# Performance work log

Hardware: AMD Instinct MI355X
Metric: run time of the kernel (lower is better)

The kernel has to match this reference:

```python
import jax, jax.numpy as jnp
import numpy as np

B, S, W = 32, 128, 16
E, CD, H, P = 256, 64, 512, 256
V, CV, NC = 50000, 256, 6
CK, WK = 8, 64  # merged char/word conv kernel sizes


def conv1d(x, w, b):
    # x: [N, Cin, L], w: [Cout, Cin, K] -> [N, Cout, L-K+1] (VALID)
    y = jax.lax.conv_general_dilated(x, w, (1,), 'VALID',
                                     dimension_numbers=('NCH', 'OIH', 'NCH'))
    return y + b[None, :, None]


def setup_inputs() -> dict:
    key = jax.random.key(0)
    ks = iter(jax.random.split(key, 40))
    nrm = lambda shape: jax.random.normal(next(ks), shape, dtype=jnp.float32) * 0.05
    return {
        'seq': jax.random.randint(next(ks), (B, S), 0, V),
        'seq_char': jax.random.randint(next(ks), (B, S, W), 0, CV),
        'classes': jnp.arange(NC, dtype=jnp.int32).reshape(NC, 1),
        'embed_w': nrm((V, E)),
        'char_embed_w': nrm((CV, CD)),
        'class_embed_w': nrm((NC, E)),
        'char_conv_w': nrm((CD, CD, CK)), 'char_conv_b': nrm((CD,)),
        'word_conv_w': nrm((E, E + CD, WK)), 'word_conv_b': nrm((E,)),
        'f_Wih': nrm((4 * H, E + CD)), 'f_Whh': nrm((4 * H, H)), 'f_b': nrm((4 * H,)),
        'b_Wih': nrm((4 * H, E + CD)), 'b_Whh': nrm((4 * H, H)), 'b_b': nrm((4 * H,)),
        'attend': nrm((E, 2 * H)),
        'd_Wih': nrm((6 * H, E + 2 * H)), 'd_Whh': nrm((6 * H, 2 * H)),
        'd_bih': nrm((6 * H,)), 'd_bhh': nrm((6 * H,)),
        'proj_w': nrm((P, 2 * H)), 'proj_b': nrm((P,)),
        'cls_w': nrm((2, P)), 'cls_b': nrm((2,)),
    }


def reference(seq, seq_char, classes, embed_w, char_embed_w, class_embed_w,
              char_conv_w, char_conv_b, word_conv_w, word_conv_b,
              f_Wih, f_Whh, f_b, b_Wih, b_Whh, b_b, attend,
              d_Wih, d_Whh, d_bih, d_bhh, proj_w, proj_b, cls_w, cls_b):
    # eval-mode forward (dropout p=0.01 is identity at eval time)
    Bq, Sq = seq.shape
    pad_mask = (seq > 0).astype(jnp.float32)            # [B,S]
    word_e = jnp.tanh(embed_w[seq])                     # [B,S,E]
    # char CNN: all char convs share kernel size -> merged into one conv
    ce = char_embed_w[seq_char]                         # [B,S,W,CD]
    ce = ce.reshape(Bq * Sq, W, CD).transpose(0, 2, 1)  # [B*S, CD, W]
    char_feat = jnp.tanh(conv1d(ce, char_conv_w, char_conv_b).mean(-1).reshape(Bq, Sq, CD))
    x = jnp.concatenate([word_e, char_feat], -1)        # [B,S,E+CD]
    # word CNN over full sequence -> [B,E]
    conv_seq = jnp.tanh(conv1d(x.transpose(0, 2, 1), word_conv_w, word_conv_b).mean(-1))
    # BiLSTM; backward direction uses seq_emb[-i], i.e. order [0, S-1, ..., 1] (as in original)
    xs = x.transpose(1, 0, 2)                           # [S,B,E+CD]
    xs_b = xs[(-jnp.arange(Sq)) % Sq]

    def lstm_scan(Wih, Whh, b, inputs):
        def step(carry, xt):
            h, c = carry
            g = xt @ Wih.T + h @ Whh.T + b
            i, f, gg, o = jnp.split(g, 4, axis=-1)
            c = jax.nn.sigmoid(f) * c + jax.nn.sigmoid(i) * jnp.tanh(gg)
            h = jax.nn.sigmoid(o) * jnp.tanh(c)
            return (h, c), h
        h0 = jnp.zeros((Bq, H), x.dtype)
        _, hs = jax.lax.scan(step, (h0, h0), inputs)
        return hs

    fouts = lstm_scan(f_Wih, f_Whh, f_b, xs)            # [S,B,H]
    bouts = lstm_scan(b_Wih, b_Whh, b_b, xs_b)[::-1]    # reversed, as in original
    seq_repr = jnp.concatenate([fouts, bouts], -1)      # [S,B,2H]
    h0 = seq_repr[-1]                                   # decoder init state [B,2H]
    seq_repr = seq_repr.transpose(1, 0, 2)              # [B,S,2H]
    # class attention: the expanded attn rows are identical across positions,
    # so sum over dim 1 of the [B,S,S] bmm equals S * tanh(a_c) . seq_repr[b,t]
    a = jnp.tanh(jnp.tanh(class_embed_w[classes[:, 0]])) @ attend   # [C,2H]
    scores = Sq * jnp.einsum('ch,bth->cbt', jnp.tanh(a), seq_repr)  # [C,B,S]
    scores = scores * pad_mask[None]
    att_ctx = jnp.einsum('cbt,bth->cbh', jnp.tanh(scores), seq_repr)  # [C,B,2H]

    def gru_step(h, ctx):
        inp = jnp.concatenate([conv_seq, ctx], -1)      # [B, E+2H]
        gi = inp @ d_Wih.T + d_bih
        gh = h @ d_Whh.T + d_bhh
        ir, iz, inn = jnp.split(gi, 3, -1)
        hr, hz, hn = jnp.split(gh, 3, -1)
        r = jax.nn.sigmoid(ir + hr)
        z = jax.nn.sigmoid(iz + hz)
        n = jnp.tanh(inn + r * hn)
        h_new = jnp.tanh((1 - z) * n + z * h)           # post-tanh state fed back (as in original)
        logits = (h_new @ proj_w.T + proj_b) @ cls_w.T + cls_b
        return h_new, jax.nn.log_softmax(logits, -1)

    _, outs = jax.lax.scan(gru_step, h0, att_ctx)       # [C,B,2]
    return outs
```

## Files before the change

kernel.cpp:

```cpp
#include <hip/hip_runtime.h>

typedef __bf16 bf16_t;
typedef __bf16 bf16x8 __attribute__((ext_vector_type(8)));
typedef float f32x4 __attribute__((ext_vector_type(4)));
typedef unsigned u32x4 __attribute__((ext_vector_type(4)));
typedef unsigned long long u64;

static constexpr int BB = 32, SS = 128, WW = 16, EE = 256, CDm = 64, HH = 512, PP = 256;
static constexpr int EC = 320;
static constexpr int H2 = 1024;
static constexpr int G6 = 3072;
static constexpr int NKT = 28;
static constexpr int NKTX = 12;

__device__ __forceinline__ float sigm(float x){ return 1.f/(1.f + expf(-x)); }

#define ALOAD(p)    __hip_atomic_load((p),  __ATOMIC_RELAXED, __HIP_MEMORY_SCOPE_AGENT)
#define ASTORE(p,v) __hip_atomic_store((p),(v),__ATOMIC_RELAXED, __HIP_MEMORY_SCOPE_AGENT)

template<bool LLC>
__device__ __forceinline__ unsigned ld_flag(const unsigned* p){
  unsigned r;
  if constexpr (LLC)
    asm volatile("global_load_dword %0, %1, off sc0 sc1\n\ts_waitcnt vmcnt(0)"
                 : "=&v"(r) : "v"(p) : "memory");
  else
    asm volatile("global_load_dword %0, %1, off sc0\n\ts_waitcnt vmcnt(0)"
                 : "=&v"(r) : "v"(p) : "memory");
  return r;
}
template<bool LLC>
__device__ __forceinline__ void ld16(u32x4& d, const void* p){
  if constexpr (LLC)
    asm volatile("global_load_dwordx4 %0, %1, off sc0 sc1" : "=&v"(d) : "v"(p) : "memory");
  else
    asm volatile("global_load_dwordx4 %0, %1, off sc0"     : "=&v"(d) : "v"(p) : "memory");
}
template<bool LLC>
__device__ __forceinline__ void st32(unsigned* p, unsigned v){
  if constexpr (LLC)
    asm volatile("global_store_dword %0, %1, off sc0 sc1" :: "v"(p), "v"(v) : "memory");
  else
    asm volatile("global_store_dword %0, %1, off sc0"     :: "v"(p), "v"(v) : "memory");
}
__device__ __forceinline__ void vm_drain(){
  asm volatile("s_waitcnt vmcnt(0)" ::: "memory");
  __builtin_amdgcn_sched_barrier(0);
}

__global__ void k_embed_cbar(const int* __restrict__ seq, const float* __restrict__ embed_w,
                             const int* __restrict__ seq_char, const float* __restrict__ cemb,
                             float* __restrict__ x, float* __restrict__ mask,
                             float* __restrict__ cbar){
  int bs = blockIdx.x; int tid = threadIdx.x;
  int wid = seq[bs];
  x[(size_t)bs*EC + tid] = tanhf(embed_w[(size_t)wid*EE + tid]);
  if (tid == 0) mask[bs] = (wid > 0) ? 1.f : 0.f;
  if (tid < 64){
    int c = tid;
    float ce[WW];
    #pragma unroll
    for (int p = 0; p < WW; ++p){
      int id = seq_char[bs*WW + p];
      ce[p] = cemb[(size_t)id*CDm + c];
    }
    #pragma unroll
    for (int k = 0; k < 8; ++k){
      float s = 0.f;
      #pragma unroll
      for (int p = 0; p < 9; ++p) s += ce[k+p];
      cbar[(size_t)bs*512 + c*8 + k] = s * (1.f/9.f);
    }
  }
}

__global__ __launch_bounds__(64) void k_xbar(const float* __restrict__ x, float* __restrict__ xbar){
  __shared__ float xl[64][129];
  int gid = blockIdx.x*64 + threadIdx.x;
  int b = gid / EC, c = gid % EC;
  int tl = threadIdx.x;
  for (int t = 0; t < SS; ++t) xl[tl][t] = x[((size_t)b*SS + t)*EC + c];
  float s = 0.f;
  for (int t = 0; t < 65; ++t) s += xl[tl][t];
  const float inv = 1.f/65.f;
  float* o = &xbar[(size_t)(b*EC + c)*64];
  o[0] = s*inv;
  for (int k = 1; k < 64; ++k){ s += xl[tl][k+64] - xl[tl][k-1]; o[k] = s*inv; }
}

template<int BM,int BN,int TM,int TN>
__global__ __launch_bounds__(256) void k_gemm(const float* __restrict__ A,
    const float* __restrict__ Wm, float* __restrict__ part,
    int M, int N, int K, int kslice){
  __shared__ float As[32][BM+4];
  __shared__ float Ws[32][BN+4];
  const int tid = threadIdx.x;
  const int tx = tid & 15, ty = tid >> 4;
  const int m0 = blockIdx.x*BM, n0 = blockIdx.y*BN, ks = blockIdx.z;
  const int kb = ks*kslice;
  float acc[TM][TN];
  #pragma unroll
  for (int i = 0; i < TM; ++i)
    #pragma unroll
    for (int j = 0; j < TN; ++j) acc[i][j] = 0.f;
  for (int kt = 0; kt < kslice; kt += 32){
    constexpr int AIT = (BM*8)/256;
    #pragma unroll
    for (int it = 0; it < AIT; ++it){
      int ch = tid + it*256;
      int r = ch >> 3, kc = (ch & 7)*4;
      float4 v = *(const float4*)(A + (size_t)(m0+r)*K + kb + kt + kc);
      As[kc+0][r]=v.x; As[kc+1][r]=v.y; As[kc+2][r]=v.z; As[kc+3][r]=v.w;
    }
    constexpr int WIT = (BN*8)/256;
    #pragma unroll
    for (int it = 0; it < WIT; ++it){
      int ch = tid + it*256;
      int r = ch >> 3, kc = (ch & 7)*4;
      float4 v = *(const float4*)(Wm + (size_t)(n0+r)*K + kb + kt + kc);
      Ws[kc+0][r]=v.x; Ws[kc+1][r]=v.y; Ws[kc+2][r]=v.z; Ws[kc+3][r]=v.w;
    }
    __syncthreads();
    #pragma unroll
    for (int kk = 0; kk < 32; ++kk){
      float a[TM], wv[TN];
      #pragma unroll
      for (int i = 0; i < TM; ++i) a[i] = As[kk][ty*TM+i];
      #pragma unroll
      for (int j = 0; j < TN; ++j) wv[j] = Ws[kk][tx*TN+j];
      #pragma unroll
      for (int i = 0; i < TM; ++i)
        #pragma unroll
        for (int j = 0; j < TN; ++j) acc[i][j] = fmaf(a[i], wv[j], acc[i][j]);
    }
    __syncthreads();
  }
  #pragma unroll
  for (int i = 0; i < TM; ++i){
    int row = m0 + ty*TM + i;
    #pragma unroll
    for (int j = 0; j < TN; ++j){
      int col = n0 + tx*TN + j;
      part[((size_t)ks*M + row)*N + col] = acc[i][j];
    }
  }
}

__global__ __launch_bounds__(256) void k_cgemm(const float* __restrict__ A,
    const float* __restrict__ Wm, const float* __restrict__ bias, float* __restrict__ x){
  __shared__ float As[32][36];
  __shared__ float Ws[32][68];
  const int tid = threadIdx.x;
  const int tx = tid & 15, ty = tid >> 4;
  const int m0 = blockIdx.x*32;
  float acc[2][4];
  #pragma unroll
  for (int i = 0; i < 2; ++i)
    #pragma unroll
    for (int j = 0; j < 4; ++j) acc[i][j] = 0.f;
  for (int kt = 0; kt < 512; kt += 32){
    {
      int r = tid >> 3, kc = (tid & 7)*4;
      float4 v = *(const float4*)(A + (size_t)(m0+r)*512 + kt + kc);
      As[kc+0][r]=v.x; As[kc+1][r]=v.y; As[kc+2][r]=v.z; As[kc+3][r]=v.w;
    }
    #pragma unroll
    for (int it = 0; it < 2; ++it){
      int ch = tid + it*256;
      int r = ch >> 3, kc = (ch & 7)*4;
      float4 v = *(const float4*)(Wm + (size_t)r*512 + kt + kc);
      Ws[kc+0][r]=v.x; Ws[kc+1][r]=v.y; Ws[kc+2][r]=v.z; Ws[kc+3][r]=v.w;
    }
    __syncthreads();
    #pragma unroll
    for (int kk = 0; kk < 32; ++kk){
      float a[2], wv[4];
      a[0] = As[kk][ty*2]; a[1] = As[kk][ty*2+1];
      #pragma unroll
      for (int j = 0; j < 4; ++j) wv[j] = Ws[kk][tx*4+j];
      #pragma unroll
      for (int i = 0; i < 2; ++i)
        #pragma unroll
        for (int j = 0; j < 4; ++j) acc[i][j] = fmaf(a[i], wv[j], acc[i][j]);
    }
    __syncthreads();
  }
  #pragma unroll
  for (int i = 0; i < 2; ++i){
    int row = m0 + ty*2 + i;
    #pragma unroll
    for (int j = 0; j < 4; ++j){
      int col = tx*4 + j;
      x[(size_t)row*EC + 256 + col] = tanhf(acc[i][j] + bias[col]);
    }
  }
}

__global__ __launch_bounds__(64) void k_fin(const float* __restrict__ part,
    const float* __restrict__ bias, float* __restrict__ out,
    int M, int N, int KS, int ldc, int act){
  int col = blockIdx.x*64 + threadIdx.x;
  int row = blockIdx.y;
  float v = bias ? bias[col] : 0.f;
  for (int ks = 0; ks < KS; ++ks) v += part[((size_t)ks*M + row)*N + col];
  if (act) v = tanhf(v);
  out[(size_t)row*ldc + col] = v;
}

__global__ __launch_bounds__(64) void k_packw(const float* __restrict__ fWih, const float* __restrict__ fWhh,
    const float* __restrict__ bWih, const float* __restrict__ bWhh, bf16_t* __restrict__ Wp){
  int id = blockIdx.x;
  int kt = id % NKT; id /= NKT;
  int slice = id % 32; int dir = id / 32;
  int l = threadIdx.x;
  const float* Whh = dir ? bWhh : fWhh;
  const float* Wih = dir ? bWih : fWih;
  int krow = (l >> 4)*8;
  for (int nt = 0; nt < 4; ++nt){
    int row = nt*512 + slice*16 + (l & 15);
    bf16_t* dst = &Wp[((((size_t)(dir*32+slice)*NKT + kt)*4 + nt)*64 + l)*8];
    if (kt < 16){
      const float* src = &Whh[(size_t)row*512 + kt*32 + krow];
      #pragma unroll
      for (int r = 0; r < 8; ++r) dst[r] = (bf16_t)src[r];
    } else {
      int kx = (kt-16)*32 + krow;
      if (kx + 8 <= 320){
        const float* src = &Wih[(size_t)row*320 + kx];
        #pragma unroll
        for (int r = 0; r < 8; ++r) dst[r] = (bf16_t)src[r];
      } else {
        #pragma unroll
        for (int r = 0; r < 8; ++r) dst[r] = (bf16_t)0.f;
      }
    }
  }
}

__global__ __launch_bounds__(64) void k_packdw(const float* __restrict__ W, bf16_t* __restrict__ Wo){
  int id = blockIdx.x;
  int kt = id % 32; id /= 32;
  int nt = id % 3;  int wg = id / 3;
  int l = threadIdx.x;
  int col = nt*1024 + wg*16 + (l & 15);
  int k0 = kt*32 + (l >> 4)*8;
  bf16_t* dst = Wo + (((size_t)(wg*3 + nt)*32 + kt)*64 + l)*8;
  const float* src = W + (size_t)col*1024 + k0;
  #pragma unroll
  for (int r = 0; r < 8; ++r) dst[r] = (bf16_t)src[r];
}

__global__ __launch_bounds__(64) void k_packpw(const float* __restrict__ W, bf16_t* __restrict__ Wo){
  int id = blockIdx.x;
  int kt = id & 31, wg = id >> 5;
  int l = threadIdx.x;
  int col = wg*16 + (l & 15);
  int k0 = kt*32 + (l >> 4)*8;
  bf16_t* dst = Wo + (((size_t)wg*32 + kt)*64 + l)*8;
  const float* src = W + (size_t)col*1024 + k0;
  #pragma unroll
  for (int r = 0; r < 8; ++r) dst[r] = (bf16_t)src[r];
}

__global__ __launch_bounds__(64) void k_packx(const float* __restrict__ x, bf16_t* __restrict__ xp){
  int id = blockIdx.x;
  int ktx = id % NKTX; id /= NKTX;
  int mt = id & 1; int t = id >> 1;
  int l = threadIdx.x;
  int b = (l & 15) + 16*mt;
  int c = ktx*32 + (l >> 4)*8;
  bf16_t* dst = &xp[(((size_t)t*2 + mt)*NKTX + ktx)*64*8 + (size_t)l*8];
  if (c + 8 <= EC){
    const float* src = &x[((size_t)b*SS + t)*EC + c];
    #pragma unroll
    for (int r = 0; r < 8; ++r) dst[r] = (bf16_t)src[r];
  } else {
    #pragma unroll
    for (int r = 0; r < 8; ++r) dst[r] = (bf16_t)0.f;
  }
}

__global__ __launch_bounds__(256) void k_zero(unsigned int* __restrict__ base, int n){
  int i = blockIdx.x*256 + threadIdx.x;
  if (i < n) ASTORE(base + i, 0u);
}

__global__ __launch_bounds__(64) void k_hprep(const float* __restrict__ seq_repr,
                                              bf16_t* __restrict__ hdp){
  int mt = blockIdx.x >> 5, kt = blockIdx.x & 31, l = threadIdx.x;
  int b = mt*16 + (l & 15);
  int jb = kt*32 + (l >> 4)*8;
  const float* src = &seq_repr[((size_t)b*SS + 127)*H2 + jb];
  unsigned* dst = (unsigned*)(hdp + (((size_t)mt*32 + kt)*64 + l)*8);
  #pragma unroll
  for (int p = 0; p < 4; ++p){
    unsigned pk = (unsigned)__builtin_bit_cast(unsigned short, (bf16_t)src[2*p])
                | ((unsigned)__builtin_bit_cast(unsigned short, (bf16_t)src[2*p+1]) << 16);
    ASTORE(dst + p, pk);
  }
}

template<bool LLC>
__device__ void lstm_body(const bf16_t* __restrict__ Wp, const bf16_t* __restrict__ xp,
    bf16_t* __restrict__ hp, const float* __restrict__ fb, const float* __restrict__ bb,
    float* __restrict__ seq_repr, unsigned* __restrict__ lf,
    int dir, int slice, int tid, bf16_t* Wl, float (*red)[32][65],
    float* bias_l, float (*c_l)[32]){
  const int wv = tid >> 6, lane = tid & 63;
  {
    const uint4* src = (const uint4*)(Wp + ((size_t)(dir*32 + slice))*NKT*4*64*8);
    uint4* dst = (uint4*)Wl;
    for (int i = tid; i < NKT*4*64*8/8; i += 256) dst[i] = src[i];
  }
  if (tid < 64){
    const float* bv = dir ? bb : fb;
    bias_l[tid] = bv[(tid >> 4)*512 + slice*16 + (tid & 15)];
  }
  ((float*)c_l)[tid]       = 0.f;
  ((float*)c_l)[tid + 256] = 0.f;
  __syncthreads();

  for (int t = 0; t < SS; ++t){
    const int ph = t & 1;
    const int s = dir ? ((SS - t) & 127) : t;
    f32x4 acc[2][4];
    f32x4 zero = {0.f,0.f,0.f,0.f};
    #pragma unroll
    for (int m = 0; m < 2; ++m)
      #pragma unroll
      for (int n = 0; n < 4; ++n) acc[m][n] = zero;

    const bf16_t* xb = xp + (size_t)s*2*NKTX*64*8;
    bf16x8 ax[3][2];
    #pragma unroll
    for (int i = 0; i < 3; ++i){
      int ktx = wv*3 + i;
      #pragma unroll
      for (int m = 0; m < 2; ++m)
        ax[i][m] = *reinterpret_cast<const bf16x8*>(xb + (((size_t)m*NKTX + ktx)*64 + lane)*8);
    }
    #pragma unroll
    for (int i = 0; i < 3; ++i){
      int kt = 16 + wv*3 + i;
      #pragma unroll
      for (int nt = 0; nt < 4; ++nt){
        bf16x8 Bf = *reinterpret_cast<const bf16x8*>(&Wl[(((size_t)kt*4 + nt)*64 + lane)*8]);
        acc[0][nt] = __builtin_amdgcn_mfma_f32_16x16x32_bf16(ax[i][0], Bf, acc[0][nt], 0, 0, 0);
        acc[1][nt] = __builtin_amdgcn_mfma_f32_16x16x32_bf16(ax[i][1], Bf, acc[1][nt], 0, 0, 0);
      }
    }
    if (t > 0 && lane < 8){
      int prod = dir*32 + (wv + 4*(lane >> 1))*2 + (lane & 1);
      const unsigned* fp = lf + prod*16;
      unsigned tgt = (unsigned)t;
      for(;;){
        unsigned v = ld_flag<LLC>(fp);
        if (__ballot(v < tgt) == 0ull) break;
      }
    }
    const bf16_t* hb_ = hp + ((size_t)(ph*2 + dir))*2*16*64*8;
    u32x4 hr[4][2];
    #pragma unroll
    for (int i = 0; i < 4; ++i){
      int kt = wv + 4*i;
      #pragma unroll
      for (int m = 0; m < 2; ++m)
        ld16<LLC>(hr[i][m], hb_ + (((size_t)m*16 + kt)*64 + lane)*8);
    }
    vm_drain();
    #pragma unroll
    for (int i = 0; i < 4; ++i){
      int kt = wv + 4*i;
      bf16x8 a0 = __builtin_bit_cast(bf16x8, hr[i][0]);
      bf16x8 a1 = __builtin_bit_cast(bf16x8, hr[i][1]);
      #pragma unroll
      for (int nt = 0; nt < 4; ++nt){
        bf16x8 Bf = *reinterpret_cast<const bf16x8*>(&Wl[(((size_t)kt*4 + nt)*64 + lane)*8]);
        acc[0][nt] = __builtin_amdgcn_mfma_f32_16x16x32_bf16(a0, Bf, acc[0][nt], 0, 0, 0);
        acc[1][nt] = __builtin_amdgcn_mfma_f32_16x16x32_bf16(a1, Bf, acc[1][nt], 0, 0, 0);
      }
    }
    {
      int r0 = (lane >> 4)*4, cc = lane & 15;
      #pragma unroll
      for (int m = 0; m < 2; ++m)
        #pragma unroll
        for (int n = 0; n < 4; ++n)
          #pragma unroll
          for (int e = 0; e < 4; ++e)
            red[wv][m*16 + r0 + e][n*16 + cc] = acc[m][n][e];
    }
    __syncthreads();
    {
      int b = tid & 31, jjp = tid >> 5;
      float hv[2];
      #pragma unroll
      for (int u2 = 0; u2 < 2; ++u2){
        int jj = jjp*2 + u2;
        float gi_ = bias_l[jj],     gf_ = bias_l[16+jj];
        float gg_ = bias_l[32+jj],  go_ = bias_l[48+jj];
        #pragma unroll
        for (int w2 = 0; w2 < 4; ++w2){
          gi_ += red[w2][b][jj];      gf_ += red[w2][b][16+jj];
          gg_ += red[w2][b][32+jj];   go_ += red[w2][b][48+jj];
        }
        float ii = sigm(gi_), ff = sigm(gf_), g2 = tanhf(gg_), oo = sigm(go_);
        float c = ff*c_l[jj][b] + ii*g2;
        c_l[jj][b] = c;
        hv[u2] = oo*tanhf(c);
      }
      int j0 = slice*16 + jjp*2;
      int s_out = dir ? (127 - t) : t;
      float2 st; st.x = hv[0]; st.y = hv[1];
      *(float2*)&seq_repr[((size_t)b*SS + s_out)*H2 + dir*HH + j0] = st;
      int mt = b >> 4, kth = j0 >> 5, ln = (b & 15) + 16*((j0 >> 3) & 3), rg = j0 & 7;
      unsigned pk = (unsigned)__builtin_bit_cast(unsigned short, (bf16_t)hv[0])
                  | ((unsigned)__builtin_bit_cast(unsigned short, (bf16_t)hv[1]) << 16);
      unsigned* dst = (unsigned*)(hp +
          ((((size_t)((ph^1)*2 + dir)*2 + mt)*16 + kth)*64 + ln)*8 + rg);
      st32<LLC>(dst, pk);
    }
    asm volatile("s_waitcnt vmcnt(0)" ::: "memory");
    __syncthreads();
    if (tid == 0)
      st32<LLC>(lf + (dir*32 + slice)*16, (unsigned)(t+1));
  }
}

__global__ __launch_bounds__(256, 1) void k_lstm(const bf16_t* __restrict__ Wp,
    const bf16_t* __restrict__ xp, bf16_t* __restrict__ hp,
    const float* __restrict__ fb, const float* __restrict__ bb,
    float* __restrict__ seq_repr, unsigned* __restrict__ lf,
    unsigned* __restrict__ xcc_tab, unsigned* __restrict__ modep){
  const int blk = blockIdx.x;
  const int tid = threadIdx.x;
  __shared__ __align__(16) bf16_t Wl[NKT*4*64*8];
  __shared__ float red[4][32][65];
  __shared__ float bias_l[64];
  __shared__ float c_l[16][32];
  __shared__ unsigned mode_s;

  unsigned xcc;
  asm volatile("s_getreg_b32 %0, hwreg(HW_REG_XCC_ID)" : "=s"(xcc));
  if (tid == 0) ASTORE(xcc_tab + blk, xcc + 1u);
  if (blk == 0){
    unsigned* tabl = (unsigned*)red;
    unsigned v = 0; int spins = 0;
    for (;;){
      v = ALOAD(xcc_tab + tid);
      if (v != 0u || spins >= 200000) break;
      ++spins; __builtin_amdgcn_s_sleep(2);
    }
    tabl[tid] = v;
    __syncthreads();
    if (tid == 0){
      unsigned mode = 1;
      unsigned c0 = tabl[0], c1 = tabl[1];
      if (c0 == 0u || c1 == 0u) mode = 2;
      for (int k = 0; k < 32; ++k)
        if (tabl[8*k] != c0 || tabl[8*k + 1] != c1) mode = 2;
      ASTORE(modep, mode);
      mode_s = mode;
    }
    __syncthreads();
  } else {
    if (tid == 0){
      unsigned m;
      while ((m = ALOAD(modep)) == 0u) __builtin_amdgcn_s_sleep(2);
      mode_s = m;
    }
    __syncthreads();
  }
  const unsigned mode = mode_s;
  int dir, slice; bool worker;
  if (mode == 1){ worker = (blk & 7) < 2; dir = blk & 7; slice = blk >> 3; }
  else          { worker = blk < 64;      dir = blk >> 5; slice = blk & 31; }
  if (!worker) return;
  if (mode == 1)
    lstm_body<false>(Wp, xp, hp, fb, bb, seq_repr, lf, dir, slice, tid, Wl, red, bias_l, c_l);
  else
    lstm_body<true >(Wp, xp, hp, fb, bb, seq_repr, lf, dir, slice, tid, Wl, red, bias_l, c_l);
}

__global__ __launch_bounds__(256) void k_ta(const int* __restrict__ classes,
    const float* __restrict__ cls_emb, const float* __restrict__ attend, float* __restrict__ ta){
  int c = blockIdx.x;
  __shared__ float t2[EE];
  int tid = threadIdx.x;
  int ci = classes[c];
  t2[tid] = tanhf(tanhf(cls_emb[(size_t)ci*EE + tid]));
  __syncthreads();
  for (int r = 0; r < 4; ++r){
    int h = r*256 + tid;
    float acc = 0.f;
    for (int e = 0; e < EE; ++e) acc = fmaf(t2[e], attend[(size_t)e*H2 + h], acc);
    ta[c*H2 + h] = tanhf(acc);
  }
}

__global__ __launch_bounds__(256) void k_ctx(const float* __restrict__ ta,
    const float* __restrict__ seq_repr, const float* __restrict__ mask, float* __restrict__ ctx){
  int c = blockIdx.x, b = blockIdx.y;
  __shared__ float ta_l[H2];
  __shared__ float ps[128][2];
  __shared__ float sc[128];
  int tid = threadIdx.x;
  for (int i = tid; i < H2; i += 256) ta_l[i] = ta[c*H2 + i];
  __syncthreads();
  {
    int tt = tid >> 1, half = tid & 1;
    const float* row = &seq_repr[((size_t)b*SS + tt)*H2 + half*512];
    const float* tl = &ta_l[half*512];
    float p = 0.f;
    for (int i = 0; i < 512; i += 4){
      float4 v = *(const float4*)&row[i];
      p = fmaf(tl[i], v.x, p);   p = fmaf(tl[i+1], v.y, p);
      p = fmaf(tl[i+2], v.z, p); p = fmaf(tl[i+3], v.w, p);
    }
    ps[tt][half] = p;
  }
  __syncthreads();
  if (tid < 128){
    float s = (ps[tid][0] + ps[tid][1]) * 128.f * mask[b*SS + tid];
    sc[tid] = tanhf(s);
  }
  __syncthreads();
  {
    int h = tid*4;
    float4 a = {0.f,0.f,0.f,0.f};
    for (int t = 0; t < SS; ++t){
      float s = sc[t];
      float4 v = *(const float4*)&seq_repr[((size_t)b*SS + t)*H2 + h];
      a.x = fmaf(s, v.x, a.x); a.y = fmaf(s, v.y, a.y);
      a.z = fmaf(s, v.z, a.z); a.w = fmaf(s, v.w, a.w);
    }
    *(float4*)&ctx[((size_t)c*BB + b)*H2 + h] = a;
  }
}

__global__ __launch_bounds__(256) void k_gemmgi(const float* __restrict__ conv_seq,
    const float* __restrict__ ctx, const float* __restrict__ Wm, float* __restrict__ part){
  __shared__ float As[32][68];
  __shared__ float Ws[32][68];
  const int tid = threadIdx.x;
  const int tx = tid & 15, ty = tid >> 4;
  const int m0 = blockIdx.x*64, n0 = blockIdx.y*64, ks = blockIdx.z;
  const int kb = ks*320;
  float acc[4][4];
  #pragma unroll
  for (int i = 0; i < 4; ++i)
    #pragma unroll
    for (int j = 0; j < 4; ++j) acc[i][j] = 0.f;
  for (int kt = 0; kt < 320; kt += 32){
    #pragma unroll
    for (int it = 0; it < 2; ++it){
      int ch = tid + it*256;
      int r = ch >> 3, kc = (ch & 7)*4;
      int row = m0 + r;
      int cc2 = row >> 5, bb2 = row & 31;
      int k4 = kb + kt + kc;
      const float* ap = (k4 < 256) ? (conv_seq + bb2*256 + k4)
                                   : (ctx + ((size_t)(cc2*BB) + bb2)*H2 + (k4 - 256));
      float4 v = *(const float4*)ap;
      As[kc+0][r]=v.x; As[kc+1][r]=v.y; As[kc+2][r]=v.z; As[kc+3][r]=v.w;
    }
    #pragma unroll
    for (int it = 0; it < 2; ++it){
      int ch = tid + it*256;
      int r = ch >> 3, kc = (ch & 7)*4;
      float4 v = *(const float4*)(Wm + (size_t)(n0+r)*1280 + kb + kt + kc);
      Ws[kc+0][r]=v.x; Ws[kc+1][r]=v.y; Ws[kc+2][r]=v.z; Ws[kc+3][r]=v.w;
    }
    __syncthreads();
    #pragma unroll
    for (int kk = 0; kk < 32; ++kk){
      float a[4], wv[4];
      #pragma unroll
      for (int i = 0; i < 4; ++i) a[i] = As[kk][ty*4+i];
      #pragma unroll
      for (int j = 0; j < 4; ++j) wv[j] = Ws[kk][tx*4+j];
      #pragma unroll
      for (int i = 0; i < 4; ++i)
        #pragma unroll
        for (int j = 0; j < 4; ++j) acc[i][j] = fmaf(a[i], wv[j], acc[i][j]);
    }
    __syncthreads();
  }
  #pragma unroll
  for (int i = 0; i < 4; ++i){
    int row = m0 + ty*4 + i;
    #pragma unroll
    for (int j = 0; j < 4; ++j){
      int col = n0 + tx*4 + j;
      part[((size_t)ks*192 + row)*G6 + col] = acc[i][j];
    }
  }
}

__global__ __launch_bounds__(256, 1) void k_dec(
    const bf16_t* __restrict__ Whp, const bf16_t* __restrict__ Ppw,
    const float* __restrict__ gi, const float* __restrict__ d_bhh,
    const float* __restrict__ seq_repr,
    const float* __restrict__ proj_b, const float* __restrict__ cls_w,
    const float* __restrict__ cls_b, bf16_t* __restrict__ hdp,
    float* __restrict__ pl, unsigned int* __restrict__ dfh,
    unsigned int* __restrict__ dfpl, float* __restrict__ out){
  const int wg = blockIdx.x;
  const int tid = threadIdx.x;
  const int wv = tid >> 6, lane = tid & 63;
  __shared__ __align__(16) bf16_t Wl[3*32*64*8];
  __shared__ float red[4][32][49];
  __shared__ float plred[8][32][2];
  __shared__ float cv[2];
  {
    const uint4* src = (const uint4*)(Whp + (size_t)wg*3*32*64*8);
    uint4* dst = (uint4*)Wl;
    for (int i = tid; i < 3*32*64*8/8; i += 256) dst[i] = src[i];
  }
  const int b = tid & 31, jp = tid >> 5;
  const int j0 = wg*16 + jp*2;
  float hold[2];
  hold[0] = seq_repr[((size_t)b*SS + 127)*H2 + j0];
  hold[1] = seq_repr[((size_t)b*SS + 127)*H2 + j0 + 1];
  float bhh[3][2];
  #pragma unroll
  for (int g = 0; g < 3; ++g){
    bhh[g][0] = d_bhh[g*1024 + j0];
    bhh[g][1] = d_bhh[g*1024 + j0 + 1];
  }
  __syncthreads();
  union HU { unsigned long long u[2]; bf16x8 v; };
  const int r0 = (lane >> 4)*4, cc = lane & 15;

  for (int c = 0; c < 6; ++c){
    if (c > 0){
      const unsigned int* fp = dfh + lane*16;
      unsigned tgt = (unsigned)c;
      for(;;){
        unsigned v = ALOAD(fp);
        if (__ballot(v < tgt) == 0ull) break;
      }
    }
    f32x4 acc[2][3];
    f32x4 zero = {0.f,0.f,0.f,0.f};
    #pragma unroll
    for (int m = 0; m < 2; ++m)
      #pragma unroll
      for (int n = 0; n < 3; ++n) acc[m][n] = zero;
    const bf16_t* hb = hdp + (size_t)(c & 1)*2*32*64*8;
    #pragma unroll
    for (int i = 0; i < 8; ++i){
      int kt = wv*8 + i;
      HU u0, u1;
      const unsigned long long* p0 = (const unsigned long long*)(hb + (((size_t)0*32 + kt)*64 + lane)*8);
      const unsigned long long* p1 = (const unsigned long long*)(hb + (((size_t)1*32 + kt)*64 + lane)*8);
      u0.u[0] = ALOAD(p0);     u0.u[1] = ALOAD(p0 + 1);
      u1.u[0] = ALOAD(p1);     u1.u[1] = ALOAD(p1 + 1);
      #pragma unroll
      for (int nt = 0; nt < 3; ++nt){
        bf16x8 Bf = *reinterpret_cast<const bf16x8*>(&Wl[(((size_t)nt*32 + kt)*64 + lane)*8]);
        acc[0][nt] = __builtin_amdgcn_mfma_f32_16x16x32_bf16(u0.v, Bf, acc[0][nt], 0, 0, 0);
        acc[1][nt] = __builtin_amdgcn_mfma_f32_16x16x32_bf16(u1.v, Bf, acc[1][nt], 0, 0, 0);
      }
    }
    #pragma unroll
    for (int m = 0; m < 2; ++m)
      #pragma unroll
      for (int n = 0; n < 3; ++n)
        #pragma unroll
        for (int e = 0; e < 4; ++e)
          red[wv][m*16 + r0 + e][n*16 + cc] = acc[m][n][e];
    __syncthreads();
    float hnew[2];
    #pragma unroll
    for (int u2 = 0; u2 < 2; ++u2){
      int jj = jp*2 + u2;
      float r_ = 0.f, z_ = 0.f, n_ = 0.f;
      #pragma unroll
      for (int w = 0; w < 4; ++w){
        r_ += red[w][b][jj]; z_ += red[w][b][16+jj]; n_ += red[w][b][32+jj];
      }
      const float* gr = gi + ((size_t)(c*BB) + b)*G6 + wg*16 + jj;
      float rr = sigm(gr[0]    + bhh[0][u2] + r_);
      float zz = sigm(gr[1024] + bhh[1][u2] + z_);
      float nn = tanhf(gr[2048] + rr*(bhh[2][u2] + n_));
      hnew[u2] = tanhf((1.f - zz)*nn + zz*hold[u2]);
      hold[u2] = hnew[u2];
    }
    {
      int kt = j0 >> 5, ln = (b & 15) + 16*((j0 >> 3) & 3), rg = j0 & 7, mt = b >> 4;
      unsigned pk = (unsigned)__builtin_bit_cast(unsigned short, (bf16_t)hnew[0])
                  | ((unsigned)__builtin_bit_cast(unsigned short, (bf16_t)hnew[1]) << 16);
      unsigned* dst = (unsigned*)(hdp + (size_t)((c+1)&1)*2*32*64*8 +
                                  (((size_t)(mt*32 + kt)*64 + ln)*8 + rg));
      ASTORE(dst, pk);
    }
    __syncthreads();
    if (tid == 0)
      ASTORE(dfh + wg*16, (unsigned)(c+1));
    if (wg < 16){
      {
        const unsigned int* fp = dfh + lane*16;
        unsigned tgt = (unsigned)(c+1);
        for(;;){
          unsigned v = ALOAD(fp);
          if (__ballot(v < tgt) == 0ull) break;
        }
      }
      f32x4 pacc[2] = {zero, zero};
      const bf16_t* hb2 = hdp + (size_t)((c+1)&1)*2*32*64*8;
      #pragma unroll
      for (int i = 0; i < 8; ++i){
        int kt = wv*8 + i;
        HU u0, u1;
        const unsigned long long* p0 = (const unsigned long long*)(hb2 + (((size_t)0*32 + kt)*64 + lane)*8);
        const unsigned long long* p1 = (const unsigned long long*)(hb2 + (((size_t)1*32 + kt)*64 + lane)*8);
        u0.u[0] = ALOAD(p0);     u0.u[1] = ALOAD(p0 + 1);
        u1.u[0] = ALOAD(p1);     u1.u[1] = ALOAD(p1 + 1);
        bf16x8 Bf = *reinterpret_cast<const bf16x8*>(Ppw + (((size_t)wg*32 + kt)*64 + lane)*8);
        pacc[0] = __builtin_amdgcn_mfma_f32_16x16x32_bf16(u0.v, Bf, pacc[0], 0, 0, 0);
        pacc[1] = __builtin_amdgcn_mfma_f32_16x16x32_bf16(u1.v, Bf, pacc[1], 0, 0, 0);
      }
      #pragma unroll
      for (int m = 0; m < 2; ++m)
        #pragma unroll
        for (int e = 0; e < 4; ++e)
          red[wv][m*16 + r0 + e][cc] = pacc[m][e];
      __syncthreads();
      {
        int colp = tid >> 5;
        float v0 = 0.f, v1 = 0.f;
        #pragma unroll
        for (int w = 0; w < 4; ++w){
          v0 += red[w][b][colp*2];
          v1 += red[w][b][colp*2+1];
        }
        int c0 = wg*16 + colp*2, c1 = c0 + 1;
        plred[colp][b][0] = v0*cls_w[c0]      + v1*cls_w[c1];
        plred[colp][b][1] = v0*cls_w[PP + c0] + v1*cls_w[PP + c1];
      }
      __syncthreads();
      if (tid < 32){
        float s0 = 0.f, s1 = 0.f;
        #pragma unroll
        for (int g = 0; g < 8; ++g){ s0 += plred[g][tid][0]; s1 += plred[g][tid][1]; }
        unsigned* dp = (unsigned*)(pl + (((size_t)c*16 + wg)*32 + tid)*2);
        ASTORE(dp,     __builtin_bit_cast(unsigned, s0));
        ASTORE(dp + 1, __builtin_bit_cast(unsigned, s1));
      }
      __syncthreads();
      if (tid == 0)
        ASTORE(dfpl + wg*16, (unsigned)(c+1));
    }
  }
  if (wg == 0){
    if (lane < 16){
      const unsigned int* fp = dfpl + lane*16;
      for(;;){
        unsigned v = ALOAD(fp);
        if (__ballot(v < 6u) == 0ull) break;
      }
    }
    __syncthreads();
    float* cr = (float*)red;
    cr[tid*2]   = proj_b[tid]*cls_w[tid];
    cr[tid*2+1] = proj_b[tid]*cls_w[PP + tid];
    __syncthreads();
    if (tid < 2){
      float s = 0.f;
      for (int i = 0; i < 256; ++i) s += cr[i*2 + tid];
      cv[tid] = s;
    }
    __syncthreads();
    if (tid < 32){
      for (int c = 0; c < 6; ++c){
        float a0 = cv[0] + cls_b[0], a1 = cv[1] + cls_b[1];
        for (int w = 0; w < 16; ++w){
          const unsigned* dp = (const unsigned*)(pl + (((size_t)c*16 + w)*32 + tid)*2);
          a0 += __builtin_bit_cast(float, ALOAD(dp));
          a1 += __builtin_bit_cast(float, ALOAD(dp + 1));
        }
        float mx = fmaxf(a0, a1);
        float ls = mx + logf(expf(a0 - mx) + expf(a1 - mx));
        out[((size_t)c*BB + tid)*2 + 0] = a0 - ls;
        out[((size_t)c*BB + tid)*2 + 1] = a1 - ls;
      }
    }
  }
}

extern "C" void kernel_launch(void* const* d_in, const int* in_sizes, int n_in,
                              void* d_out, int out_size, void* d_ws, size_t ws_size,
                              hipStream_t stream){
  const int*   seq          = (const int*)  d_in[0];
  const int*   seq_char     = (const int*)  d_in[1];
  const int*   classes      = (const int*)  d_in[2];
  const float* embed_w      = (const float*)d_in[3];
  const float* char_embed_w = (const float*)d_in[4];
  const float* class_embed_w= (const float*)d_in[5];
  const float* char_conv_w  = (const float*)d_in[6];
  const float* char_conv_b  = (const float*)d_in[7];
  const float* word_conv_w  = (const float*)d_in[8];
  const float* word_conv_b  = (const float*)d_in[9];
  const float* f_Wih = (const float*)d_in[10];
  const float* f_Whh = (const float*)d_in[11];
  const float* f_b   = (const float*)d_in[12];
  const float* b_Wih = (const float*)d_in[13];
  const float* b_Whh = (const float*)d_in[14];
  const float* b_b   = (const float*)d_in[15];
  const float* attend = (const float*)d_in[16];
  const float* d_Wih  = (const float*)d_in[17];
  const float* d_Whh  = (const float*)d_in[18];
  const float* d_bih  = (const float*)d_in[19];
  const float* d_bhh  = (const float*)d_in[20];
  const float* proj_w = (const float*)d_in[21];
  const float* proj_b = (const float*)d_in[22];
  const float* cls_w  = (const float*)d_in[23];
  const float* cls_b  = (const float*)d_in[24];
  float* out = (float*)d_out;

  char* wsb = (char*)d_ws;
  size_t off = 0;
  auto alloc = [&](size_t bytes) -> char* {
    char* p = wsb + off;
    off += (bytes + 255) & ~(size_t)255;
    return p;
  };
  unsigned int* flags = (unsigned int*)alloc(12288);
  unsigned int* lf   = flags;
  unsigned int* dfh  = flags + 1024;
  unsigned int* dfpl = flags + 2048;
  unsigned int* xcc_tab = (unsigned int*)alloc(1024);
  unsigned int* modep   = (unsigned int*)alloc(256);
  bf16_t* hp  = (bf16_t*)alloc((size_t)2*2*2*16*64*8 * 2);
  const int ZERO_DWORDS = 3072 + 256 + 64 + 32768;
  bf16_t* hdp = (bf16_t*)alloc((size_t)2*2*32*64*8 * 2);
  bf16_t* Wp  = (bf16_t*)alloc((size_t)2*32*NKT*4*64*8 * 2);
  bf16_t* Whp = (bf16_t*)alloc((size_t)64*3*32*64*8 * 2);
  bf16_t* Ppw = (bf16_t*)alloc((size_t)16*32*64*8 * 2);
  bf16_t* xp  = (bf16_t*)alloc((size_t)128*2*NKTX*64*8 * 2);
  float* pl       = (float*)alloc((size_t)6*16*32*2*4);
  float* x        = (float*)alloc((size_t)BB*SS*EC*4);
  float* mask     = (float*)alloc((size_t)BB*SS*4);
  float* cbar     = (float*)alloc((size_t)4096*512*4);
  float* xbar     = (float*)alloc((size_t)BB*EC*64*4);
  float* conv_seq = (float*)alloc((size_t)BB*256*4);
  float* seq_repr = (float*)alloc((size_t)BB*SS*H2*4);
  float* ta       = (float*)alloc((size_t)6*H2*4);
  float* ctx      = (float*)alloc((size_t)6*BB*H2*4);
  float* inp      = (float*)alloc((size_t)192*1280*4);
  float* gi       = (float*)alloc((size_t)192*G6*4);
  float* part_char= (float*)alloc((size_t)2*4096*64*4);
  float* part_word= (float*)alloc((size_t)32*BB*256*4);
  float* part_gi  = (float*)alloc((size_t)4*192*G6*4);
  (void)ws_size; (void)in_sizes; (void)n_in; (void)out_size;
  (void)inp; (void)part_char;

  k_zero<<<(ZERO_DWORDS + 255)/256, 256, 0, stream>>>((unsigned int*)d_ws, ZERO_DWORDS);

  k_packw<<<2*32*NKT, 64, 0, stream>>>(f_Wih, f_Whh, b_Wih, b_Whh, Wp);
  k_packdw<<<64*3*32, 64, 0, stream>>>(d_Whh, Whp);
  k_packpw<<<16*32, 64, 0, stream>>>(proj_w, Ppw);
  k_embed_cbar<<<BB*SS, 256, 0, stream>>>(seq, embed_w, seq_char, char_embed_w, x, mask, cbar);
  k_cgemm<<<128, 256, 0, stream>>>(cbar, char_conv_w, char_conv_b, x);
  k_xbar<<<160, 64, 0, stream>>>(x, xbar);
  k_gemm<32,64,2,4><<<dim3(1,4,32), 256, 0, stream>>>(xbar, word_conv_w, part_word, 32, 256, 20480, 640);
  k_fin<<<dim3(4,32), 64, 0, stream>>>(part_word, word_conv_b, conv_seq, 32, 256, 32, 256, 1);
  k_packx<<<128*2*NKTX, 64, 0, stream>>>(x, xp);
  k_lstm<<<256, 256, 0, stream>>>(Wp, xp, hp, f_b, b_b, seq_repr, lf, xcc_tab, modep);
  k_ta<<<6, 256, 0, stream>>>(classes, class_embed_w, attend, ta);
  k_ctx<<<dim3(6,32), 256, 0, stream>>>(ta, seq_repr, mask, ctx);
  k_gemmgi<<<dim3(3,48,4), 256, 0, stream>>>(conv_seq, ctx, d_Wih, part_gi);
  k_fin<<<dim3(48,192), 64, 0, stream>>>(part_gi, d_bih, gi, 192, G6, 4, G6, 0);
  k_hprep<<<64, 64, 0, stream>>>(seq_repr, hdp);
  k_dec<<<64, 256, 0, stream>>>(Whp, Ppw, gi, d_bhh, seq_repr, proj_b, cls_w, cls_b,
                                hdp, pl, dfh, dfpl, out);
}
```

Before: 646.7 us.

## Merge prep kernels, fold ta and hprep into LSTM, use fast sigmoid/tanh

Combines the zeroing and three weight-packing kernels into one launch. Moves the class-attention vector computation into otherwise idle blocks of the LSTM kernel, and has the LSTM write the final decoder hidden state directly, removing two more launches. It also reorders the LSTM step so the step flag is published before the fp32 seq_repr store, shortening the critical path, and swaps in __expf-based sigmoid/tanh in the LSTM and GRU steps. The risks are small accuracy loss from the fast math and the ordering between the hdp stores and the decoder.

```diff
diff --git a/kernel.cpp b/kernel.cpp
--- a/kernel.cpp
+++ b/kernel.cpp
@@ -14,6 +14,8 @@
 static constexpr int NKTX = 12;
 
 __device__ __forceinline__ float sigm(float x){ return 1.f/(1.f + expf(-x)); }
+__device__ __forceinline__ float fsigm(float x){ return 1.f/(1.f + __expf(-x)); }
+__device__ __forceinline__ float ftanh(float x){ return 1.f - 2.f/(1.f + __expf(2.f*x)); }
 
 #define ALOAD(p)    __hip_atomic_load((p),  __ATOMIC_RELAXED, __HIP_MEMORY_SCOPE_AGENT)
 #define ASTORE(p,v) __hip_atomic_store((p),(v),__ATOMIC_RELAXED, __HIP_MEMORY_SCOPE_AGENT)
@@ -207,59 +209,63 @@
   out[(size_t)row*ldc + col] = v;
 }
 
-__global__ __launch_bounds__(64) void k_packw(const float* __restrict__ fWih, const float* __restrict__ fWhh,
-    const float* __restrict__ bWih, const float* __restrict__ bWhh, bf16_t* __restrict__ Wp){
-  int id = blockIdx.x;
-  int kt = id % NKT; id /= NKT;
-  int slice = id % 32; int dir = id / 32;
+__global__ __launch_bounds__(64) void k_prep(
+    const float* __restrict__ fWih, const float* __restrict__ fWhh,
+    const float* __restrict__ bWih, const float* __restrict__ bWhh, bf16_t* __restrict__ Wp,
+    const float* __restrict__ dWhh, bf16_t* __restrict__ Whp,
+    const float* __restrict__ projw, bf16_t* __restrict__ Ppw,
+    unsigned int* __restrict__ zbase, int nzero){
+  int blk = blockIdx.x;
   int l = threadIdx.x;
-  const float* Whh = dir ? bWhh : fWhh;
-  const float* Wih = dir ? bWih : fWih;
-  int krow = (l >> 4)*8;
-  for (int nt = 0; nt < 4; ++nt){
-    int row = nt*512 + slice*16 + (l & 15);
-    bf16_t* dst = &Wp[((((size_t)(dir*32+slice)*NKT + kt)*4 + nt)*64 + l)*8];
-    if (kt < 16){
-      const float* src = &Whh[(size_t)row*512 + kt*32 + krow];
-      #pragma unroll
-      for (int r = 0; r < 8; ++r) dst[r] = (bf16_t)src[r];
-    } else {
-      int kx = (kt-16)*32 + krow;
-      if (kx + 8 <= 320){
-        const float* src = &Wih[(size_t)row*320 + kx];
+  if (blk < 1792){
+    int id = blk;
+    int kt = id % NKT; id /= NKT;
+    int slice = id % 32; int dir = id / 32;
+    const float* Whh = dir ? bWhh : fWhh;
+    const float* Wih = dir ? bWih : fWih;
+    int krow = (l >> 4)*8;
+    for (int nt = 0; nt < 4; ++nt){
+      int row = nt*512 + slice*16 + (l & 15);
+      bf16_t* dst = &Wp[((((size_t)(dir*32+slice)*NKT + kt)*4 + nt)*64 + l)*8];
+      if (kt < 16){
+        const float* src = &Whh[(size_t)row*512 + kt*32 + krow];
         #pragma unroll
         for (int r = 0; r < 8; ++r) dst[r] = (bf16_t)src[r];
       } else {
-        #pragma unroll
-        for (int r = 0; r < 8; ++r) dst[r] = (bf16_t)0.f;
-      }
-    }
-  }
-}
-
-__global__ __launch_bounds__(64) void k_packdw(const float* __restrict__ W, bf16_t* __restrict__ Wo){
-  int id = blockIdx.x;
-  int kt = id % 32; id /= 32;
-  int nt = id % 3;  int wg = id / 3;
-  int l = threadIdx.x;
-  int col = nt*1024 + wg*16 + (l & 15);
-  int k0 = kt*32 + (l >> 4)*8;
-  bf16_t* dst = Wo + (((size_t)(wg*3 + nt)*32 + kt)*64 + l)*8;
-  const float* src = W + (size_t)col*1024 + k0;
-  #pragma unroll
-  for (int r = 0; r < 8; ++r) dst[r] = (bf16_t)src[r];
-}
-
-__global__ __launch_bounds__(64) void k_packpw(const float* __restrict__ W, bf16_t* __restrict__ Wo){
-  int id = blockIdx.x;
-  int kt = id & 31, wg = id >> 5;
-  int l = threadIdx.x;
-  int col = wg*16 + (l & 15);
-  int k0 = kt*32 + (l >> 4)*8;
-  bf16_t* dst = Wo + (((size_t)wg*32 + kt)*64 + l)*8;
-  const float* src = W + (size_t)col*1024 + k0;
-  #pragma unroll
-  for (int r = 0; r < 8; ++r) dst[r] = (bf16_t)src[r];
+        int kx = (kt-16)*32 + krow;
+        if (kx + 8 <= 320){
+          const float* src = &Wih[(size_t)row*320 + kx];
+          #pragma unroll
+          for (int r = 0; r < 8; ++r) dst[r] = (bf16_t)src[r];
+        } else {
+          #pragma unroll
+          for (int r = 0; r < 8; ++r) dst[r] = (bf16_t)0.f;
+        }
+      }
+    }
+  } else if (blk < 7936){
+    int id = blk - 1792;
+    int kt = id % 32; id /= 32;
+    int nt = id % 3;  int wg = id / 3;
+    int col = nt*1024 + wg*16 + (l & 15);
+    int k0 = kt*32 + (l >> 4)*8;
+    bf16_t* dst = Whp + (((size_t)(wg*3 + nt)*32 + kt)*64 + l)*8;
+    const float* src = dWhh + (size_t)col*1024 + k0;
+    #pragma unroll
+    for (int r = 0; r < 8; ++r) dst[r] = (bf16_t)src[r];
+  } else if (blk < 8448){
+    int id = blk - 7936;
+    int kt = id & 31, wg = id >> 5;
+    int col = wg*16 + (l & 15);
+    int k0 = kt*32 + (l >> 4)*8;
+    bf16_t* dst = Ppw + (((size_t)wg*32 + kt)*64 + l)*8;
+    const float* src = projw + (size_t)col*1024 + k0;
+    #pragma unroll
+    for (int r = 0; r < 8; ++r) dst[r] = (bf16_t)src[r];
+  } else {
+    int i = (blk - 8448)*64 + l;
+    if (i < nzero) ASTORE(zbase + i, 0u);
+  }
 }
 
 __global__ __launch_bounds__(64) void k_packx(const float* __restrict__ x, bf16_t* __restrict__ xp){
@@ -280,30 +286,10 @@
   }
 }
 
-__global__ __launch_bounds__(256) void k_zero(unsigned int* __restrict__ base, int n){
-  int i = blockIdx.x*256 + threadIdx.x;
-  if (i < n) ASTORE(base + i, 0u);
-}
-
-__global__ __launch_bounds__(64) void k_hprep(const float* __restrict__ seq_repr,
-                                              bf16_t* __restrict__ hdp){
-  int mt = blockIdx.x >> 5, kt = blockIdx.x & 31, l = threadIdx.x;
-  int b = mt*16 + (l & 15);
-  int jb = kt*32 + (l >> 4)*8;
-  const float* src = &seq_repr[((size_t)b*SS + 127)*H2 + jb];
-  unsigned* dst = (unsigned*)(hdp + (((size_t)mt*32 + kt)*64 + l)*8);
-  #pragma unroll
-  for (int p = 0; p < 4; ++p){
-    unsigned pk = (unsigned)__builtin_bit_cast(unsigned short, (bf16_t)src[2*p])
-                | ((unsigned)__builtin_bit_cast(unsigned short, (bf16_t)src[2*p+1]) << 16);
-    ASTORE(dst + p, pk);
-  }
-}
-
 template<bool LLC>
 __device__ void lstm_body(const bf16_t* __restrict__ Wp, const bf16_t* __restrict__ xp,
     bf16_t* __restrict__ hp, const float* __restrict__ fb, const float* __restrict__ bb,
-    float* __restrict__ seq_repr, unsigned* __restrict__ lf,
+    float* __restrict__ seq_repr, unsigned* __restrict__ lf, bf16_t* __restrict__ hdp,
     int dir, int slice, int tid, bf16_t* Wl, float (*red)[32][65],
     float* bias_l, float (*c_l)[32]){
   const int wv = tid >> 6, lane = tid & 63;
@@ -391,39 +377,45 @@
             red[wv][m*16 + r0 + e][n*16 + cc] = acc[m][n][e];
     }
     __syncthreads();
+    const int b = tid & 31, jjp = tid >> 5;
+    float hv[2];
+    #pragma unroll
+    for (int u2 = 0; u2 < 2; ++u2){
+      int jj = jjp*2 + u2;
+      float gi_ = bias_l[jj],     gf_ = bias_l[16+jj];
+      float gg_ = bias_l[32+jj],  go_ = bias_l[48+jj];
+      #pragma unroll
+      for (int w2 = 0; w2 < 4; ++w2){
+        gi_ += red[w2][b][jj];      gf_ += red[w2][b][16+jj];
+        gg_ += red[w2][b][32+jj];   go_ += red[w2][b][48+jj];
+      }
+      float ii = fsigm(gi_), ff = fsigm(gf_), g2 = ftanh(gg_), oo = fsigm(go_);
+      float c = ff*c_l[jj][b] + ii*g2;
+      c_l[jj][b] = c;
+      hv[u2] = oo*ftanh(c);
+    }
+    const int j0 = slice*16 + jjp*2;
+    unsigned pk = (unsigned)__builtin_bit_cast(unsigned short, (bf16_t)hv[0])
+                | ((unsigned)__builtin_bit_cast(unsigned short, (bf16_t)hv[1]) << 16);
     {
-      int b = tid & 31, jjp = tid >> 5;
-      float hv[2];
-      #pragma unroll
-      for (int u2 = 0; u2 < 2; ++u2){
-        int jj = jjp*2 + u2;
-        float gi_ = bias_l[jj],     gf_ = bias_l[16+jj];
-        float gg_ = bias_l[32+jj],  go_ = bias_l[48+jj];
-        #pragma unroll
-        for (int w2 = 0; w2 < 4; ++w2){
-          gi_ += red[w2][b][jj];      gf_ += red[w2][b][16+jj];
-          gg_ += red[w2][b][32+jj];   go_ += red[w2][b][48+jj];
-        }
-        float ii = sigm(gi_), ff = sigm(gf_), g2 = tanhf(gg_), oo = sigm(go_);
-        float c = ff*c_l[jj][b] + ii*g2;
-        c_l[jj][b] = c;
-        hv[u2] = oo*tanhf(c);
-      }
-      int j0 = slice*16 + jjp*2;
+      int mt = b >> 4, kth = j0 >> 5, ln = (b & 15) + 16*((j0 >> 3) & 3), rg = j0 & 7;
+      unsigned* dst = (unsigned*)(hp +
+          ((((size_t)((ph^1)*2 + dir)*2 + mt)*16 + kth)*64 + ln)*8 + rg);
+      st32<LLC>(dst, pk);
+      if ((dir == 0 && t == 127) || (dir == 1 && t == 0)){
+        int ktd = dir*16 + kth;
+        ASTORE((unsigned*)(hdp + (((size_t)(mt*32 + ktd)*64 + ln)*8 + rg)), pk);
+      }
+    }
+    asm volatile("s_waitcnt vmcnt(0)" ::: "memory");
+    __syncthreads();
+    if (tid == 0)
+      st32<LLC>(lf + (dir*32 + slice)*16, (unsigned)(t+1));
+    {
       int s_out = dir ? (127 - t) : t;
       float2 st; st.x = hv[0]; st.y = hv[1];
       *(float2*)&seq_repr[((size_t)b*SS + s_out)*H2 + dir*HH + j0] = st;
-      int mt = b >> 4, kth = j0 >> 5, ln = (b & 15) + 16*((j0 >> 3) & 3), rg = j0 & 7;
-      unsigned pk = (unsigned)__builtin_bit_cast(unsigned short, (bf16_t)hv[0])
-                  | ((unsigned)__builtin_bit_cast(unsigned short, (bf16_t)hv[1]) << 16);
-      unsigned* dst = (unsigned*)(hp +
-          ((((size_t)((ph^1)*2 + dir)*2 + mt)*16 + kth)*64 + ln)*8 + rg);
-      st32<LLC>(dst, pk);
-    }
-    asm volatile("s_waitcnt vmcnt(0)" ::: "memory");
-    __syncthreads();
-    if (tid == 0)
-      st32<LLC>(lf + (dir*32 + slice)*16, (unsigned)(t+1));
+    }
   }
 }
 
@@ -431,7 +423,10 @@
     const bf16_t* __restrict__ xp, bf16_t* __restrict__ hp,
     const float* __restrict__ fb, const float* __restrict__ bb,
     float* __restrict__ seq_repr, unsigned* __restrict__ lf,
-    unsigned* __restrict__ xcc_tab, unsigned* __restrict__ modep){
+    unsigned* __restrict__ xcc_tab, unsigned* __restrict__ modep,
+    bf16_t* __restrict__ hdp,
+    const int* __restrict__ classes, const float* __restrict__ cls_emb,
+    const float* __restrict__ attend, float* __restrict__ ta){
   const int blk = blockIdx.x;
   const int tid = threadIdx.x;
   __shared__ __align__(16) bf16_t Wl[NKT*4*64*8];
@@ -475,27 +470,28 @@
   int dir, slice; bool worker;
   if (mode == 1){ worker = (blk & 7) < 2; dir = blk & 7; slice = blk >> 3; }
   else          { worker = blk < 64;      dir = blk >> 5; slice = blk & 31; }
-  if (!worker) return;
+  if (!worker){
+    bool ta_blk; int c;
+    if (mode == 1){ ta_blk = ((blk & 7) == 2) && ((blk >> 3) < 6); c = blk >> 3; }
+    else          { ta_blk = (blk >= 64 && blk < 70);              c = blk - 64; }
+    if (ta_blk){
+      float* t2 = (float*)red;
+      int ci = classes[c];
+      t2[tid] = tanhf(tanhf(cls_emb[(size_t)ci*EE + tid]));
+      __syncthreads();
+      for (int r = 0; r < 4; ++r){
+        int h = r*256 + tid;
+        float a2 = 0.f;
+        for (int e = 0; e < EE; ++e) a2 = fmaf(t2[e], attend[(size_t)e*H2 + h], a2);
+        ta[c*H2 + h] = tanhf(a2);
+      }
+    }
+    return;
+  }
   if (mode == 1)
-    lstm_body<false>(Wp, xp, hp, fb, bb, seq_repr, lf, dir, slice, tid, Wl, red, bias_l, c_l);
+    lstm_body<false>(Wp, xp, hp, fb, bb, seq_repr, lf, hdp, dir, slice, tid, Wl, red, bias_l, c_l);
   else
-    lstm_body<true >(Wp, xp, hp, fb, bb, seq_repr, lf, dir, slice, tid, Wl, red, bias_l, c_l);
-}
-
-__global__ __launch_bounds__(256) void k_ta(const int* __restrict__ classes,
-    const float* __restrict__ cls_emb, const float* __restrict__ attend, float* __restrict__ ta){
-  int c = blockIdx.x;
-  __shared__ float t2[EE];
-  int tid = threadIdx.x;
-  int ci = classes[c];
-  t2[tid] = tanhf(tanhf(cls_emb[(size_t)ci*EE + tid]));
-  __syncthreads();
-  for (int r = 0; r < 4; ++r){
-    int h = r*256 + tid;
-    float acc = 0.f;
-    for (int e = 0; e < EE; ++e) acc = fmaf(t2[e], attend[(size_t)e*H2 + h], acc);
-    ta[c*H2 + h] = tanhf(acc);
-  }
+    lstm_body<true >(Wp, xp, hp, fb, bb, seq_repr, lf, hdp, dir, slice, tid, Wl, red, bias_l, c_l);
 }
 
 __global__ __launch_bounds__(256) void k_ctx(const float* __restrict__ ta,
@@ -681,10 +677,10 @@
         r_ += red[w][b][jj]; z_ += red[w][b][16+jj]; n_ += red[w][b][32+jj];
       }
       const float* gr = gi + ((size_t)(c*BB) + b)*G6 + wg*16 + jj;
-      float rr = sigm(gr[0]    + bhh[0][u2] + r_);
-      float zz = sigm(gr[1024] + bhh[1][u2] + z_);
-      float nn = tanhf(gr[2048] + rr*(bhh[2][u2] + n_));
-      hnew[u2] = tanhf((1.f - zz)*nn + zz*hold[u2]);
+      float rr = fsigm(gr[0]    + bhh[0][u2] + r_);
+      float zz = fsigm(gr[1024] + bhh[1][u2] + z_);
+      float nn = ftanh(gr[2048] + rr*(bhh[2][u2] + n_));
+      hnew[u2] = ftanh((1.f - zz)*nn + zz*hold[u2]);
       hold[u2] = hnew[u2];
     }
     {
@@ -856,23 +852,20 @@
   (void)ws_size; (void)in_sizes; (void)n_in; (void)out_size;
   (void)inp; (void)part_char;
 
-  k_zero<<<(ZERO_DWORDS + 255)/256, 256, 0, stream>>>((unsigned int*)d_ws, ZERO_DWORDS);
-
-  k_packw<<<2*32*NKT, 64, 0, stream>>>(f_Wih, f_Whh, b_Wih, b_Whh, Wp);
-  k_packdw<<<64*3*32, 64, 0, stream>>>(d_Whh, Whp);
-  k_packpw<<<16*32, 64, 0, stream>>>(proj_w, Ppw);
+  k_prep<<<9013, 64, 0, stream>>>(f_Wih, f_Whh, b_Wih, b_Whh, Wp,
+                                  d_Whh, Whp, proj_w, Ppw,
+                                  (unsigned int*)d_ws, ZERO_DWORDS);
   k_embed_cbar<<<BB*SS, 256, 0, stream>>>(seq, embed_w, seq_char, char_embed_w, x, mask, cbar);
   k_cgemm<<<128, 256, 0, stream>>>(cbar, char_conv_w, char_conv_b, x);
   k_xbar<<<160, 64, 0, stream>>>(x, xbar);
   k_gemm<32,64,2,4><<<dim3(1,4,32), 256, 0, stream>>>(xbar, word_conv_w, part_word, 32, 256, 20480, 640);
   k_fin<<<dim3(4,32), 64, 0, stream>>>(part_word, word_conv_b, conv_seq, 32, 256, 32, 256, 1);
   k_packx<<<128*2*NKTX, 64, 0, stream>>>(x, xp);
-  k_lstm<<<256, 256, 0, stream>>>(Wp, xp, hp, f_b, b_b, seq_repr, lf, xcc_tab, modep);
-  k_ta<<<6, 256, 0, stream>>>(classes, class_embed_w, attend, ta);
+  k_lstm<<<256, 256, 0, stream>>>(Wp, xp, hp, f_b, b_b, seq_repr, lf, xcc_tab, modep,
+                                  hdp, classes, class_embed_w, attend, ta);
   k_ctx<<<dim3(6,32), 256, 0, stream>>>(ta, seq_repr, mask, ctx);
   k_gemmgi<<<dim3(3,48,4), 256, 0, stream>>>(conv_seq, ctx, d_Wih, part_gi);
   k_fin<<<dim3(48,192), 64, 0, stream>>>(part_gi, d_bih, gi, 192, G6, 4, G6, 0);
-  k_hprep<<<64, 64, 0, stream>>>(seq_repr, hdp);
   k_dec<<<64, 256, 0, stream>>>(Whp, Ppw, gi, d_bhh, seq_repr, proj_b, cls_w, cls_b,
                                 hdp, pl, dfh, dfpl, out);
 }
```

Result: faster. 576.0 us (-10.9%).
